# Kernel tuning notes

Measured on AMD Instinct MI355X. Metric: run time of the kernel, lower is better.

Reference implementation:

```python
import jax, jax.numpy as jnp
import numpy as np

D = 1024; H = 16; DKV = 64; DFF = 4096
NB = 32; MAXD = 128
B = 4; LD = 1024; LE = 1024
NEG = -1e9
EPS = 1e-6


def setup_inputs():
    key = jax.random.key(0)
    ks = jax.random.split(key, 13)
    s = 0.02
    def W(k, shape):
        return jax.random.normal(k, shape, jnp.float32) * s
    return {
        "encoder_hidden_states": jax.random.normal(ks[0], (B, LE, D), jnp.float32),
        "hidden_states": jax.random.normal(ks[1], (B, LD, D), jnp.float32),
        "ln1_w": jnp.ones((D,), jnp.float32),
        "sa_q": W(ks[2], (D, H * DKV)),
        "sa_k": W(ks[3], (D, H * DKV)),
        "sa_v": W(ks[4], (D, H * DKV)),
        "sa_o": W(ks[5], (H * DKV, D)),
        "rel_bias": W(ks[6], (NB, H)),
        "ln2_w": jnp.ones((D,), jnp.float32),
        "ca_q": W(ks[7], (D, H * DKV)),
        "ca_k": W(ks[8], (D, H * DKV)),
        "ca_v": W(ks[9], (D, H * DKV)),
        "ca_o": W(ks[10], (H * DKV, D)),
        "ln3_w": jnp.ones((D,), jnp.float32),
        "wi": W(ks[11], (D, DFF)),
        "wo": W(ks[12], (DFF, D)),
        "final_ln_w": jnp.ones((D,), jnp.float32),
        "encoder_attention_mask": jnp.ones((B, LE), jnp.int32),
        "attention_mask": jnp.ones((B, LD), jnp.int32),
    }


def _rms(x, w):
    # T5 LayerNorm: RMS norm, no mean subtraction, no bias
    var = jnp.mean(x * x, axis=-1, keepdims=True)
    return x * jax.lax.rsqrt(var + EPS) * w


def _rel_bucket(rp):
    # T5 relative position bucketing, non-bidirectional (decoder causal)
    n = -jnp.minimum(rp, 0)
    max_exact = NB // 2
    is_small = n < max_exact
    nf = jnp.maximum(n, 1).astype(jnp.float32)
    val_large = max_exact + (
        jnp.log(nf / max_exact) / np.log(MAXD / max_exact) * (NB - max_exact)
    ).astype(jnp.int32)
    val_large = jnp.minimum(val_large, NB - 1)
    return jnp.where(is_small, n, val_large)


def _attn(xq, xkv, Wq, Wk, Wv, Wo, bias):
    b, lq, _ = xq.shape
    lk = xkv.shape[1]
    q = (xq @ Wq).reshape(b, lq, H, DKV)
    k = (xkv @ Wk).reshape(b, lk, H, DKV)
    v = (xkv @ Wv).reshape(b, lk, H, DKV)
    # T5: no 1/sqrt(d) scaling; additive position bias + mask before softmax
    scores = jnp.einsum('bqhd,bkhd->bhqk', q, k) + bias
    p = jax.nn.softmax(scores, axis=-1)
    o = jnp.einsum('bhqk,bkhd->bqhd', p, v).reshape(b, lq, H * DKV)
    return o @ Wo


def reference(encoder_hidden_states, hidden_states, ln1_w, sa_q, sa_k, sa_v, sa_o,
              rel_bias, ln2_w, ca_q, ca_k, ca_v, ca_o, ln3_w, wi, wo, final_ln_w,
              encoder_attention_mask, attention_mask):
    b, ld, _ = hidden_states.shape
    q_pos = jnp.arange(ld)[:, None]
    k_pos = jnp.arange(ld)[None, :]
    pos_bias = rel_bias[_rel_bucket(k_pos - q_pos)].transpose(2, 0, 1)[None]  # [1,H,LD,LD]
    # decoder extended mask: causal AND padding
    self_ok = (k_pos <= q_pos)[None, None] & (attention_mask[:, None, None, :] > 0)
    self_bias = pos_bias + jnp.where(self_ok, 0.0, NEG)
    # cross-attention: encoder padding mask; enc-dec position bias is zeros
    cross_bias = jnp.where(encoder_attention_mask[:, None, None, :] > 0, 0.0, NEG)

    h = hidden_states
    x = _rms(h, ln1_w)
    h = h + _attn(x, x, sa_q, sa_k, sa_v, sa_o, self_bias)
    x = _rms(h, ln2_w)
    h = h + _attn(x, encoder_hidden_states, ca_q, ca_k, ca_v, ca_o, cross_bias)
    x = _rms(h, ln3_w)
    h = h + jax.nn.relu(x @ wi) @ wo
    return _rms(h, final_ln_w)
```

## Files before the change

kernel.cpp:

```cpp
#include <hip/hip_runtime.h>


#define BB   4
#define LDEC 1024
#define LENC 1024
#define DIM  1024
#define NH   16
#define DK   64
#define DFFN 4096
#define NEGF (-1e9f)

typedef unsigned short u16;
typedef __attribute__((ext_vector_type(8))) unsigned short u16x8;
typedef __attribute__((ext_vector_type(8))) short s16x8;
typedef __attribute__((ext_vector_type(4))) float f32x4;

__device__ __forceinline__ float bf2f(u16 u) {
    union { unsigned int i; float f; } c; c.i = ((unsigned int)u) << 16; return c.f;
}
__device__ __forceinline__ u16 f2bf(float f) {
    union { float f; unsigned int i; } c; c.f = f;
    unsigned int x = c.i;
    return (u16)((x + 0x7fffu + ((x >> 16) & 1u)) >> 16);
}
__device__ __forceinline__ bool probe_f32(const void* probe) {
    return ((const u16*)probe)[0] != 0x3F80;
}
__device__ __forceinline__ float ldx(const void* p, long i, bool f32) {
    return f32 ? ((const float*)p)[i] : bf2f(((const u16*)p)[i]);
}
__device__ __forceinline__ float4 ldx4(const void* p, long i, bool f32) {
    if (f32) return ((const float4*)p)[i >> 2];
    ushort4 u = ((const ushort4*)p)[i >> 2];
    return make_float4(bf2f(u.x), bf2f(u.y), bf2f(u.z), bf2f(u.w));
}
__device__ __forceinline__ void stx(void* p, long i, float v, bool f32) {
    if (f32) ((float*)p)[i] = v;
    else     ((u16*)p)[i] = f2bf(v);
}

__device__ __forceinline__ void gload16(const void* g, void* l) {
    __builtin_amdgcn_global_load_lds(
        (const __attribute__((address_space(1))) void*)g,
        (__attribute__((address_space(3))) void*)l, 16, 0, 0);
}

__global__ __launch_bounds__(256) void copy_k(const void* __restrict__ src,
                                              void* __restrict__ dst,
                                              const void* __restrict__ probe, int n) {
    bool pf = probe_f32(probe);
    long bytes = (long)n * (pf ? 4 : 2);
    long off = ((long)blockIdx.x * 256 + threadIdx.x) * 16;
    if (off < bytes)
        *(int4*)((char*)dst + off) = *(const int4*)((const char*)src + off);
}

__global__ __launch_bounds__(256) void cvt_k(const void* __restrict__ src,
                                             u16* __restrict__ dst,
                                             const void* __restrict__ probe, int n4) {
    bool pf = probe_f32(probe);
    int i = blockIdx.x * 256 + threadIdx.x;
    if (i >= n4) return;
    if (pf) {
        float4 f = ((const float4*)src)[i];
        ushort4 o;
        o.x = f2bf(f.x); o.y = f2bf(f.y); o.z = f2bf(f.z); o.w = f2bf(f.w);
        ((ushort4*)dst)[i] = o;
    } else {
        ((ushort4*)dst)[i] = ((const ushort4*)src)[i];
    }
}

struct TPack {
    const void* s[10]; void* d[10];
    int K[10], N[10], t0[11];
};
__global__ __launch_bounds__(256) void transp_k(TPack p, const void* __restrict__ probe) {
    bool pf = probe_f32(probe);
    __shared__ u16 tl[32][33];
    int bid = blockIdx.x;
    int w = 0;
    while (bid >= p.t0[w + 1]) ++w;
    int lt = bid - p.t0[w];
    const int K = p.K[w], N = p.N[w];
    const int ntx = N >> 5;
    const int bn = (lt % ntx) * 32, bk = (lt / ntx) * 32;
    const int c = threadIdx.x & 31, rr = threadIdx.x >> 5;
    const void* s = p.s[w];
    u16* d = (u16*)p.d[w];
#pragma unroll
    for (int i = 0; i < 4; ++i) {
        int r = rr + i * 8;
        long gi = (long)(bk + r) * N + bn + c;
        tl[c][r] = pf ? f2bf(((const float*)s)[gi]) : ((const u16*)s)[gi];
    }
    __syncthreads();
#pragma unroll
    for (int i = 0; i < 4; ++i) {
        int r = rr + i * 8;
        d[(long)(bn + r) * K + bk + c] = tl[r][c];
    }
}

template <int XM, int YM, int CP, int AD>
__global__ __launch_bounds__(256) void rms_k(const void* __restrict__ X,
                                             const void* __restrict__ w,
                                             void* __restrict__ Y,
                                             void* __restrict__ R,
                                             const u16* __restrict__ G,
                                             const u16* __restrict__ G2,
                                             const void* __restrict__ probe,
                                             long xoff, long yoff) {
    bool pf = probe_f32(probe);
    bool xf = XM && pf, yf = YM && pf;
    const int row = blockIdx.x, t = threadIdx.x;
    const long idx = (long)row * DIM + t * 4;
    float4 xv = ldx4(X, xoff + idx, xf);
    if (AD >= 1) {
        float4 gv = ldx4(G, idx, false);
        xv.x += gv.x; xv.y += gv.y; xv.z += gv.z; xv.w += gv.w;
    }
    if (AD >= 2) {
        float4 gv = ldx4(G2, idx, false);
        xv.x += gv.x; xv.y += gv.y; xv.z += gv.z; xv.w += gv.w;
    }
    float ss = xv.x * xv.x;
    ss = fmaf(xv.y, xv.y, ss);
    ss = fmaf(xv.z, xv.z, ss);
    ss = fmaf(xv.w, xv.w, ss);
#pragma unroll
    for (int off = 32; off; off >>= 1) ss += __shfl_xor(ss, off, 64);
    __shared__ float part[4];
    if ((t & 63) == 0) part[t >> 6] = ss;
    __syncthreads();
    float tot = part[0] + part[1] + part[2] + part[3];
    float scale = rsqrtf(tot * (1.f / (float)DIM) + 1e-6f);
    float4 wv = ldx4(w, t * 4, pf);
    if (CP) {
        stx(R, idx + 0, xv.x, pf);
        stx(R, idx + 1, xv.y, pf);
        stx(R, idx + 2, xv.z, pf);
        stx(R, idx + 3, xv.w, pf);
    }
    stx(Y, yoff + idx + 0, xv.x * scale * wv.x, yf);
    stx(Y, yoff + idx + 1, xv.y * scale * wv.y, yf);
    stx(Y, yoff + idx + 2, xv.z * scale * wv.z, yf);
    stx(Y, yoff + idx + 3, xv.w * scale * wv.w, yf);
}

struct Gemm2Arg {
    const u16* A; const u16* BT; void* C;
    long aoff; long boff; long coff; int ldb; int klen;
};

template <int EPI, int BM>
__global__ __launch_bounds__(512) void mgemm2_k(Gemm2Arg g0, Gemm2Arg g1, Gemm2Arg g2,
                                                const void* __restrict__ probe,
                                                int M, int N, int K) {
    const bool pf = probe_f32(probe);
    Gemm2Arg ga = (blockIdx.z == 0) ? g0 : (blockIdx.z == 1 ? g1 : g2);
    constexpr int AG = BM / 64;
    constexpr int AFR = BM / 32;

    __shared__ u16 Asm[2][BM * 64];
    __shared__ u16 Bsm[2][128 * 64];

    const int tid = threadIdx.x;
    const int nx = gridDim.x;
    const int nwg = nx * gridDim.y;
    const int L = blockIdx.x + nx * blockIdx.y;
    const int tile = (L & 7) * (nwg >> 3) + (L >> 3);
    const int m_base = (tile / nx) * BM, n_base = (tile % nx) * 128;

    const int w = tid >> 6, lane = tid & 63;
    const int wm = w >> 2, wn = w & 3;
    const int l15 = lane & 15, quad = lane >> 4;
    const int arow8 = lane >> 3;
    const int acg = (lane & 7) ^ arow8;

    const int iters = ga.klen >> 6;
    const u16* Ab = ga.A + ga.aoff;
    const u16* Bb = ga.BT + ga.boff;

#pragma unroll
    for (int g = 0; g < AG; ++g)
        gload16(Ab + (long)(m_base + w * (BM / 8) + g * 8 + arow8) * K + acg * 8,
                &Asm[0][(w * (BM / 8) + g * 8) * 64]);
#pragma unroll
    for (int g = 0; g < 2; ++g)
        gload16(Bb + (long)(n_base + w * 16 + g * 8 + arow8) * ga.ldb + acg * 8,
                &Bsm[0][(w * 16 + g * 8) * 64]);

    f32x4 acc[AFR][2] = {};
    int cur = 0;
    for (int it = 0; it < iters; ++it) {
        __syncthreads();
        if (it + 1 < iters) {
            const int k0 = (it + 1) << 6;
#pragma unroll
            for (int g = 0; g < AG; ++g)
                gload16(Ab + (long)(m_base + w * (BM / 8) + g * 8 + arow8) * K + k0 + acg * 8,
                        &Asm[cur ^ 1][(w * (BM / 8) + g * 8) * 64]);
#pragma unroll
            for (int g = 0; g < 2; ++g)
                gload16(Bb + (long)(n_base + w * 16 + g * 8 + arow8) * ga.ldb + k0 + acg * 8,
                        &Bsm[cur ^ 1][(w * 16 + g * 8) * 64]);
        }
#pragma unroll
        for (int s = 0; s < 2; ++s) {
            s16x8 afr[AFR], bfr[2];
#pragma unroll
            for (int i = 0; i < AFR; ++i) {
                int row = wm * (BM / 2) + i * 16 + l15;
                int chunk = ((s << 2) | quad) ^ (row & 7);
                afr[i] = *(const s16x8*)&Asm[cur][row * 64 + chunk * 8];
            }
#pragma unroll
            for (int j = 0; j < 2; ++j) {
                int nr = wn * 32 + j * 16 + l15;
                int chunk = ((s << 2) | quad) ^ (nr & 7);
                bfr[j] = *(const s16x8*)&Bsm[cur][nr * 64 + chunk * 8];
            }
#pragma unroll
            for (int i = 0; i < AFR; ++i)
#pragma unroll
                for (int j = 0; j < 2; ++j)
                    acc[i][j] = __builtin_amdgcn_mfma_f32_16x16x32_bf16(
                        afr[i], bfr[j], acc[i][j], 0, 0, 0);
        }
        cur ^= 1;
    }

#pragma unroll
    for (int i = 0; i < AFR; ++i) {
#pragma unroll
        for (int j = 0; j < 2; ++j) {
            int n = n_base + wn * 32 + j * 16 + l15;
#pragma unroll
            for (int r4 = 0; r4 < 4; ++r4) {
                int m = m_base + wm * (BM / 2) + i * 16 + quad * 4 + r4;
                float v = acc[i][j][r4];
                if (EPI == 1) v = fmaxf(v, 0.f);
                long cidx = ga.coff + (long)m * N + n;
                if (EPI == 2) {
                    v += ldx(ga.C, cidx, pf);
                    stx(ga.C, cidx, v, pf);
                } else {
                    ((u16*)ga.C)[cidx] = f2bf(v);
                }
            }
        }
    }
}

struct GemmArg {
    const void* A; const void* B; void* C;
    long aoff; long boff; long coff; int asrc; int bsrc; int ldb;
};

__device__ __forceinline__ void load_breg(const GemmArg& ga, bool bf, int k0,
                                          int bk2, int bnb, int n_base, u16* breg) {
    long base0 = (long)(k0 + bk2) * ga.ldb + ga.boff + n_base + bnb;
    long base1 = base0 + ga.ldb;
    if (bf) {
        const float4* Bf = (const float4*)ga.B;
#pragma unroll
        for (int r = 0; r < 2; ++r) {
            long b = (r ? base1 : base0) >> 2;
#pragma unroll
            for (int c = 0; c < 2; ++c) {
                float4 f = Bf[b + c];
                breg[r * 8 + c * 4 + 0] = f2bf(f.x);
                breg[r * 8 + c * 4 + 1] = f2bf(f.y);
                breg[r * 8 + c * 4 + 2] = f2bf(f.z);
                breg[r * 8 + c * 4 + 3] = f2bf(f.w);
            }
        }
    } else {
        u16x8 v0 = *(const u16x8*)((const u16*)ga.B + base0);
        u16x8 v1 = *(const u16x8*)((const u16*)ga.B + base1);
#pragma unroll
        for (int i = 0; i < 8; ++i) { breg[i] = v0[i]; breg[8 + i] = v1[i]; }
    }
}

template <int EPI>
__global__ __launch_bounds__(512) void mgemm_k(GemmArg g0, GemmArg g1, GemmArg g2,
                                               const void* __restrict__ probe,
                                               int M, int N, int K) {
    const bool pf = probe_f32(probe);
    GemmArg ga = (blockIdx.z == 0) ? g0 : (blockIdx.z == 1 ? g1 : g2);
    const bool af = (ga.asrc >= 1) && pf;
    const bool bf = (ga.bsrc >= 1) && pf;

    __shared__ u16 Asm[2][128 * 64];
    __shared__ u16 Bsm[128 * 64];

    const int tid = threadIdx.x;
    const int nx = gridDim.x;
    const int nwg = nx * gridDim.y;
    const int L = blockIdx.x + nx * blockIdx.y;
    const int tile = (L & 7) * (nwg >> 3) + (L >> 3);
    const int m_base = (tile / nx) * 128, n_base = (tile % nx) * 128;

    const int w = tid >> 6, lane = tid & 63;
    const int wm = w >> 2, wn = w & 3;
    const int l15 = lane & 15, quad = lane >> 4;

    const int bk2 = (tid & 31) * 2;
    const int bnb = (tid >> 5) * 8;
    const int arow8 = lane >> 3;
    const int acg = (lane & 7) ^ arow8;

    const int iters = K >> 6;
    u16 breg[16];
    load_breg(ga, bf, 0, bk2, bnb, n_base, breg);
    if (!af) {
#pragma unroll
        for (int g = 0; g < 2; ++g) {
            const u16* Ag = (const u16*)ga.A + ga.aoff +
                            (long)(m_base + w * 16 + g * 8 + arow8) * K + acg * 8;
            gload16(Ag, &Asm[0][(w * 16 + g * 8) * 64]);
        }
    }

    f32x4 acc[4][2] = {};

    for (int it = 0; it < iters; ++it) {
        const int cur = it & 1;
        __syncthreads();
        if (af) {
            const int row = tid >> 2;
            const float4* Af = (const float4*)ga.A;
            long gb = ga.aoff + (long)(m_base + row) * K + (it << 6);
#pragma unroll
            for (int c = 0; c < 2; ++c) {
                int cg = (tid & 3) * 2 + c;
                float4 fa = Af[(gb + cg * 8) >> 2];
                float4 fb = Af[((gb + cg * 8) >> 2) + 1];
                u16x8 o;
                o[0] = f2bf(fa.x); o[1] = f2bf(fa.y); o[2] = f2bf(fa.z); o[3] = f2bf(fa.w);
                o[4] = f2bf(fb.x); o[5] = f2bf(fb.y); o[6] = f2bf(fb.z); o[7] = f2bf(fb.w);
                *(u16x8*)&Asm[cur][row * 64 + ((cg ^ (row & 7)) << 3)] = o;
            }
        }
#pragma unroll
        for (int i = 0; i < 8; ++i) {
            int n = bnb + i;
            unsigned int pr = (unsigned int)breg[i] | ((unsigned int)breg[8 + i] << 16);
            *(unsigned int*)&Bsm[n * 64 + (((bk2 >> 3) ^ (n & 7)) << 3) + (bk2 & 7)] = pr;
        }
        __syncthreads();
        if (it + 1 < iters) {
            load_breg(ga, bf, (it + 1) << 6, bk2, bnb, n_base, breg);
            if (!af) {
#pragma unroll
                for (int g = 0; g < 2; ++g) {
                    const u16* Ag = (const u16*)ga.A + ga.aoff +
                                    (long)(m_base + w * 16 + g * 8 + arow8) * K +
                                    ((it + 1) << 6) + acg * 8;
                    gload16(Ag, &Asm[cur ^ 1][(w * 16 + g * 8) * 64]);
                }
            }
        }
#pragma unroll
        for (int s = 0; s < 2; ++s) {
            s16x8 afr[4], bfr[2];
#pragma unroll
            for (int i = 0; i < 4; ++i) {
                int row = wm * 64 + i * 16 + l15;
                int chunk = ((s << 2) | quad) ^ (row & 7);
                afr[i] = *(const s16x8*)&Asm[cur][row * 64 + chunk * 8];
            }
#pragma unroll
            for (int j = 0; j < 2; ++j) {
                int nr = wn * 32 + j * 16 + l15;
                int chunk = ((s << 2) | quad) ^ (nr & 7);
                bfr[j] = *(const s16x8*)&Bsm[nr * 64 + chunk * 8];
            }
#pragma unroll
            for (int i = 0; i < 4; ++i)
#pragma unroll
                for (int j = 0; j < 2; ++j)
                    acc[i][j] = __builtin_amdgcn_mfma_f32_16x16x32_bf16(
                        afr[i], bfr[j], acc[i][j], 0, 0, 0);
        }
    }

#pragma unroll
    for (int i = 0; i < 4; ++i) {
#pragma unroll
        for (int j = 0; j < 2; ++j) {
            int n = n_base + wn * 32 + j * 16 + l15;
#pragma unroll
            for (int r4 = 0; r4 < 4; ++r4) {
                int m = m_base + wm * 64 + i * 16 + quad * 4 + r4;
                float v = acc[i][j][r4];
                if (EPI == 1) v = fmaxf(v, 0.f);
                long cidx = ga.coff + (long)m * N + n;
                if (EPI == 2) {
                    v += ldx(ga.C, cidx, pf);
                    stx(ga.C, cidx, v, pf);
                } else {
                    ((u16*)ga.C)[cidx] = f2bf(v);
                }
            }
        }
    }
}

template <int SELF>
__global__ __launch_bounds__(256) void fattn_k(const u16* __restrict__ Q,
                                               const u16* __restrict__ K,
                                               const u16* __restrict__ V,
                                               const void* __restrict__ relb,
                                               const int* __restrict__ mask,
                                               u16* __restrict__ O,
                                               const void* __restrict__ probe,
                                               int LK, int b0, int bufrows) {
    const bool pf = probe_f32(probe);
    __shared__ u16 Ks[64][72];
    __shared__ u16 Vt[64][72];
    __shared__ u16 Ps[64][72];
    __shared__ float bias_lut[SELF ? 1024 : 1];

    const int t = threadIdx.x;
    const int lane = t & 63, w = t >> 6;
    const int l15 = lane & 15, quad = lane >> 4;

    int x, h, z;
    if (gridDim.z == 4) {
        int lid = blockIdx.x + (int)gridDim.x * (blockIdx.y + (int)gridDim.y * blockIdx.z);
        int q = lid >> 8, r = lid & 255, a = r & 3;
        x = (q == 0) ? a : (q == 1) ? 15 - a : (q == 2) ? 4 + a : 11 - a;
        h = (r >> 2) & 15;
        z = r >> 6;
    } else {
        x = blockIdx.x; h = blockIdx.y; z = blockIdx.z;
    }
    const int q0 = x * 64;
    const int batch = b0 + z;
    const long bv = (long)z * bufrows * DIM;
    const int* mrow = mask + batch * LK;

    if (SELF) {
        for (int i = t; i < 1024; i += 256) {
            int bucket;
            if (i < 16) bucket = i;
            else {
                int vv = 16 + (int)(logf((float)i * 0.0625f) * 7.69436394f);
                bucket = vv < 31 ? vv : 31;
            }
            bias_lut[i] = ldx(relb, bucket * NH + h, pf);
        }
    }

    s16x8 qf[2];
    {
        const u16* qp = Q + bv + (long)(q0 + w * 16 + l15) * DIM + h * DK + quad * 8;
        qf[0] = *(const s16x8*)qp;
        qf[1] = *(const s16x8*)(qp + 32);
    }

    float l_reg[4] = {0.f, 0.f, 0.f, 0.f};
    f32x4 Oa[4] = {};

    const int ntiles = SELF ? (q0 >> 6) + 1 : (LK >> 6);
    const int kr = t >> 2, kseg = t & 3;
    const int kr2 = (t & 31) * 2, dnb = (t >> 5) * 8;

    u16x8 kp0, kp1, vp0, vp1;
    {
        long gb = bv + (long)kr * DIM + h * DK + kseg * 16;
        kp0 = *(const u16x8*)(K + gb);
        kp1 = *(const u16x8*)(K + gb + 8);
        long gv = bv + (long)kr2 * DIM + h * DK + dnb;
        vp0 = *(const u16x8*)(V + gv);
        vp1 = *(const u16x8*)(V + gv + DIM);
    }

    for (int kt = 0; kt < ntiles; ++kt) {
        __syncthreads();
        *(u16x8*)&Ks[kr][kseg * 16] = kp0;
        *(u16x8*)&Ks[kr][kseg * 16 + 8] = kp1;
#pragma unroll
        for (int i = 0; i < 8; ++i) {
            unsigned int pr = (unsigned int)vp0[i] | ((unsigned int)vp1[i] << 16);
            *(unsigned int*)&Vt[dnb + i][kr2] = pr;
        }
        __syncthreads();
        if (kt + 1 < ntiles) {
            long gb = bv + (long)((kt + 1) * 64 + kr) * DIM + h * DK + kseg * 16;
            kp0 = *(const u16x8*)(K + gb);
            kp1 = *(const u16x8*)(K + gb + 8);
            long gv = bv + (long)((kt + 1) * 64 + kr2) * DIM + h * DK + dnb;
            vp0 = *(const u16x8*)(V + gv);
            vp1 = *(const u16x8*)(V + gv + DIM);
        }

        f32x4 sc[4] = {};
        __builtin_amdgcn_s_setprio(1);
#pragma unroll
        for (int j = 0; j < 4; ++j)
#pragma unroll
            for (int s = 0; s < 2; ++s) {
                s16x8 bf = *(const s16x8*)&Ks[j * 16 + l15][s * 32 + quad * 8];
                sc[j] = __builtin_amdgcn_mfma_f32_16x16x32_bf16(qf[s], bf, sc[j], 0, 0, 0);
            }
        __builtin_amdgcn_s_setprio(0);

#pragma unroll
        for (int j = 0; j < 4; ++j) {
            int key = kt * 64 + j * 16 + l15;
            float ma = (mrow[key] > 0) ? 0.f : NEGF;
#pragma unroll
            for (int r = 0; r < 4; ++r) {
                float sv = sc[j][r];
                if (SELF) {
                    int q = q0 + w * 16 + quad * 4 + r;
                    int d = q - key;
                    sv += bias_lut[d < 0 ? 0 : d] + ((key <= q) ? ma : NEGF);
                } else {
                    sv += ma;
                }
                float p = __expf(sv);
                Ps[w * 16 + quad * 4 + r][j * 16 + l15] = f2bf(p);
                l_reg[r] += p;
            }
        }
        asm volatile("" ::: "memory");

        __builtin_amdgcn_s_setprio(1);
#pragma unroll
        for (int s = 0; s < 2; ++s) {
            s16x8 pa = *(const s16x8*)&Ps[w * 16 + l15][s * 32 + quad * 8];
#pragma unroll
            for (int j = 0; j < 4; ++j) {
                s16x8 vb = *(const s16x8*)&Vt[j * 16 + l15][s * 32 + quad * 8];
                Oa[j] = __builtin_amdgcn_mfma_f32_16x16x32_bf16(pa, vb, Oa[j], 0, 0, 0);
            }
        }
        __builtin_amdgcn_s_setprio(0);
    }

#pragma unroll
    for (int r = 0; r < 4; ++r) {
        float v = l_reg[r];
        v += __shfl_xor(v, 1, 64);
        v += __shfl_xor(v, 2, 64);
        v += __shfl_xor(v, 4, 64);
        v += __shfl_xor(v, 8, 64);
        l_reg[r] = 1.f / v;
    }
#pragma unroll
    for (int j = 0; j < 4; ++j)
#pragma unroll
        for (int r = 0; r < 4; ++r) {
            int row = w * 16 + quad * 4 + r;
            O[bv + (long)(q0 + row) * DIM + h * DK + j * 16 + l15] =
                f2bf(Oa[j][r] * l_reg[r]);
        }
}

extern "C" void kernel_launch(void* const* d_in, const int* in_sizes, int n_in,
                              void* d_out, int out_size, void* d_ws, size_t ws_size,
                              hipStream_t stream) {
    const void* enc  = d_in[0];
    const void* hs   = d_in[1];
    const void* ln1  = d_in[2];
    const void* sa_q = d_in[3];
    const void* sa_k = d_in[4];
    const void* sa_v = d_in[5];
    const void* sa_o = d_in[6];
    const void* relb = d_in[7];
    const void* ln2  = d_in[8];
    const void* ca_q = d_in[9];
    const void* ca_k = d_in[10];
    const void* ca_v = d_in[11];
    const void* ca_o = d_in[12];
    const void* ln3  = d_in[13];
    const void* wi   = d_in[14];
    const void* wo   = d_in[15];
    const void* fln  = d_in[16];
    const int* enc_mask = (const int*)d_in[17];
    const int* dec_mask = (const int*)d_in[18];
    void* out = d_out;
    const void* probe = ln1;

    char* ws = (char*)d_ws;
    const int M = BB * LDEC;
    dim3 blk(256), blkG(512);
    GemmArg dz = {nullptr, nullptr, nullptr, 0, 0, 0, 0, 0, 0};
    Gemm2Arg dz2 = {nullptr, nullptr, nullptr, 0, 0, 0, 0, 0};

    if (ws_size >= (72ull << 20)) {
        u16* X0 = (u16*)(ws);
        u16* X1 = (u16*)(ws + (8u  << 20));
        u16* X2 = (u16*)(ws + (16u << 20));
        u16* X3 = (u16*)(ws + (24u << 20));
        u16* FF = X1;
        u16* encB = (u16*)(ws + (32u << 20));
        u16* G3b = (u16*)(ws + (40u << 20));
        u16* wT[10];
        wT[0] = (u16*)(ws + (40u << 20));
        wT[1] = (u16*)(ws + (42u << 20));
        wT[2] = (u16*)(ws + (44u << 20));
        wT[3] = (u16*)(ws + (46u << 20));
        wT[4] = (u16*)(ws + (48u << 20));
        wT[5] = (u16*)(ws + (50u << 20));
        wT[6] = (u16*)(ws + (52u << 20));
        wT[7] = (u16*)(ws + (54u << 20));
        wT[8] = (u16*)(ws + (56u << 20));
        wT[9] = (u16*)(ws + (64u << 20));

        cvt_k<<<4096, blk, 0, stream>>>(enc, encB, probe, 1048576);
        {
            TPack p;
            const void* s[10] = {sa_q, sa_k, sa_v, sa_o, ca_q, ca_k, ca_v, ca_o, wi, wo};
            const int kk[10] = {DIM, DIM, DIM, DIM, DIM, DIM, DIM, DIM, DIM, DFFN};
            const int nn[10] = {DIM, DIM, DIM, DIM, DIM, DIM, DIM, DIM, DFFN, DIM};
            int acc = 0;
            for (int i = 0; i < 10; ++i) {
                p.s[i] = s[i]; p.d[i] = wT[i]; p.K[i] = kk[i]; p.N[i] = nn[i];
                p.t0[i] = acc; acc += (kk[i] >> 5) * (nn[i] >> 5);
            }
            p.t0[10] = acc;
            transp_k<<<acc, blk, 0, stream>>>(p, probe);
        }

        dim3 gQKV(8, 64, 3);
        dim3 gOP2(8, 64, 2);
        dim3 gWI(16, 64, 2);
        dim3 gAttn(LDEC / 64, NH, BB);

        rms_k<1, 0, 1, 0><<<M, blk, 0, stream>>>(hs, ln1, X0, out, nullptr, nullptr,
                                                 probe, 0, 0);
        {
            Gemm2Arg zq = {X0, wT[0], X1, 0, 0, 0, DIM, DIM};
            Gemm2Arg zk = {X0, wT[1], X2, 0, 0, 0, DIM, DIM};
            Gemm2Arg zv = {X0, wT[2], X3, 0, 0, 0, DIM, DIM};
            mgemm2_k<0, 64><<<gQKV, blkG, 0, stream>>>(zq, zk, zv, probe, M, DIM, DIM);
        }
        fattn_k<1><<<gAttn, blk, 0, stream>>>(X1, X2, X3, relb, dec_mask, X0,
                                              probe, LDEC, 0, LDEC);
        {
            Gemm2Arg za = {X0, wT[3], X1, 0, 0, 0, DIM, 512};
            Gemm2Arg zb = {X0, wT[3], X2, 512, 512, 0, DIM, 512};
            mgemm2_k<0, 64><<<gOP2, blkG, 0, stream>>>(za, zb, dz2, probe, M, DIM, DIM);
        }

        rms_k<1, 0, 1, 2><<<M, blk, 0, stream>>>(out, ln2, X0, out, X1, X2,
                                                 probe, 0, 0);
        {
            Gemm2Arg zq = {X0, wT[4], X1, 0, 0, 0, DIM, DIM};
            Gemm2Arg zk = {encB, wT[5], X2, 0, 0, 0, DIM, DIM};
            Gemm2Arg zv = {encB, wT[6], X3, 0, 0, 0, DIM, DIM};
            mgemm2_k<0, 64><<<gQKV, blkG, 0, stream>>>(zq, zk, zv, probe, M, DIM, DIM);
        }
        fattn_k<0><<<gAttn, blk, 0, stream>>>(X1, X2, X3, relb, enc_mask, X0,
                                              probe, LENC, 0, LENC);
        {
            Gemm2Arg za = {X0, wT[7], X1, 0, 0, 0, DIM, 512};
            Gemm2Arg zb = {X0, wT[7], X2, 512, 512, 0, DIM, 512};
            mgemm2_k<0, 64><<<gOP2, blkG, 0, stream>>>(za, zb, dz2, probe, M, DIM, DIM);
        }

        rms_k<1, 0, 1, 2><<<M, blk, 0, stream>>>(out, ln3, X0, out, X1, X2,
                                                 probe, 0, 0);
        {
            Gemm2Arg z0 = {X0, wT[8], FF, 0, 0, 0, DIM, DIM};
            Gemm2Arg z1 = {X0, wT[8], FF, 0, (long)2048 * DIM, 2048, DIM, DIM};
            mgemm2_k<1, 64><<<gWI, blkG, 0, stream>>>(z0, z1, dz2, probe, M, DFFN, DIM);
        }
        {
            Gemm2Arg za = {FF, wT[9], X0, 0, 0, 0, DFFN, 2048};
            Gemm2Arg zb = {FF, wT[9], G3b, 2048, 2048, 0, DFFN, 2048};
            mgemm2_k<0, 64><<<gOP2, blkG, 0, stream>>>(za, zb, dz2, probe, M, DIM, DFFN);
        }

        rms_k<1, 1, 0, 2><<<M, blk, 0, stream>>>(out, fln, out, nullptr, X0, G3b,
                                                 probe, 0, 0);
    } else if (ws_size >= (32ull << 20)) {
        u16* X0 = (u16*)(ws);
        u16* X1 = (u16*)(ws + (8u << 20));
        u16* X2 = (u16*)(ws + (16u << 20));
        u16* X3 = (u16*)(ws + (24u << 20));
        u16* FF = X2;
        const bool have_encb = ws_size >= (40ull << 20);
        u16* encB = (u16*)(ws + (32u << 20));

        dim3 gQKV(8, 32, 3);
        dim3 gOP(8, 32, 1);
        dim3 gWI(16, 32, 1);
        dim3 gAttn(LDEC / 64, NH, BB);

        copy_k<<<(M * DIM / 4) / 256, blk, 0, stream>>>(hs, out, probe, M * DIM);
        if (have_encb)
            cvt_k<<<4096, blk, 0, stream>>>(enc, encB, probe, M * DIM / 4);

        rms_k<1, 0, 0, 0><<<M, blk, 0, stream>>>(out, ln1, X0, nullptr, nullptr, nullptr, probe, 0, 0);
        {
            GemmArg zq = {X0, sa_q, X1, 0, 0, 0, 0, 1, DIM};
            GemmArg zk = {X0, sa_k, X2, 0, 0, 0, 0, 1, DIM};
            GemmArg zv = {X0, sa_v, X3, 0, 0, 0, 0, 1, DIM};
            mgemm_k<0><<<gQKV, blkG, 0, stream>>>(zq, zk, zv, probe, M, DIM, DIM);
        }
        fattn_k<1><<<gAttn, blk, 0, stream>>>(X1, X2, X3, relb, dec_mask, X0,
                                              probe, LDEC, 0, LDEC);
        {
            GemmArg zo = {X0, sa_o, out, 0, 0, 0, 0, 1, DIM};
            mgemm_k<2><<<gOP, blkG, 0, stream>>>(zo, dz, dz, probe, M, DIM, DIM);
        }

        rms_k<1, 0, 0, 0><<<M, blk, 0, stream>>>(out, ln2, X0, nullptr, nullptr, nullptr, probe, 0, 0);
        {
            const void* encA = have_encb ? (const void*)encB : enc;
            int asrc = have_encb ? 0 : 1;
            GemmArg zq = {X0, ca_q, X1, 0, 0, 0, 0, 1, DIM};
            GemmArg zk = {encA, ca_k, X2, 0, 0, 0, asrc, 1, DIM};
            GemmArg zv = {encA, ca_v, X3, 0, 0, 0, asrc, 1, DIM};
            mgemm_k<0><<<gQKV, blkG, 0, stream>>>(zq, zk, zv, probe, M, DIM, DIM);
        }
        fattn_k<0><<<gAttn, blk, 0, stream>>>(X1, X2, X3, relb, enc_mask, X0,
                                              probe, LENC, 0, LENC);
        {
            GemmArg zo = {X0, ca_o, out, 0, 0, 0, 0, 1, DIM};
            mgemm_k<2><<<gOP, blkG, 0, stream>>>(zo, dz, dz, probe, M, DIM, DIM);
        }

        rms_k<1, 0, 0, 0><<<M, blk, 0, stream>>>(out, ln3, X0, nullptr, nullptr, nullptr, probe, 0, 0);
        for (int d = 0; d < 2; ++d) {
            GemmArg zi = {X0, wi, FF, 0, (long)d * 2048, 0, 0, 1, DFFN};
            mgemm_k<1><<<gWI, blkG, 0, stream>>>(zi, dz, dz, probe, M, 2048, DIM);
            GemmArg zo = {FF, wo, out, 0, (long)d * 2048 * DIM, 0, 0, 1, DIM};
            mgemm_k<2><<<gOP, blkG, 0, stream>>>(zo, dz, dz, probe, M, DIM, 2048);
        }
        rms_k<1, 1, 0, 0><<<M, blk, 0, stream>>>(out, fln, out, nullptr, nullptr, nullptr, probe, 0, 0);
        return;
    } else {
        u16* X0 = (u16*)(ws);
        u16* X1 = (u16*)(ws + (2u << 20));
        u16* X2 = (u16*)(ws + (4u << 20));
        u16* X3 = (u16*)(ws + (6u << 20));
        u16* XN = (u16*)(ws);
        u16* FF = (u16*)(ws + (4u << 20));
        dim3 gQKV(8, 8, 3);
        dim3 gOP(8, 8, 1);
        dim3 gFFN(8, 16, 1);
        dim3 gAttn(LDEC / 64, NH, 1);

        copy_k<<<(M * DIM / 4) / 256, blk, 0, stream>>>(hs, out, probe, M * DIM);

        for (int b = 0; b < BB; ++b) {
            const long ob = (long)b * LDEC * DIM;
            const long eb = (long)b * LENC * DIM;

            rms_k<1, 0, 0, 0><<<LDEC, blk, 0, stream>>>(out, ln1, X0, nullptr, nullptr, nullptr, probe, ob, 0);
            {
                GemmArg zq = {X0, sa_q, X1, 0, 0, 0, 0, 1, DIM};
                GemmArg zk = {X0, sa_k, X2, 0, 0, 0, 0, 1, DIM};
                GemmArg zv = {X0, sa_v, X3, 0, 0, 0, 0, 1, DIM};
                mgemm_k<0><<<gQKV, blkG, 0, stream>>>(zq, zk, zv, probe, LDEC, DIM, DIM);
            }
            fattn_k<1><<<gAttn, blk, 0, stream>>>(X1, X2, X3, relb, dec_mask, X0,
                                                  probe, LDEC, b, 0);
            {
                GemmArg zo = {X0, sa_o, out, 0, 0, ob, 0, 1, DIM};
                mgemm_k<2><<<gOP, blkG, 0, stream>>>(zo, dz, dz, probe, LDEC, DIM, DIM);
            }

            rms_k<1, 0, 0, 0><<<LDEC, blk, 0, stream>>>(out, ln2, X0, nullptr, nullptr, nullptr, probe, ob, 0);
            {
                GemmArg zq = {X0, ca_q, X1, 0, 0, 0, 0, 1, DIM};
                GemmArg zk = {enc, ca_k, X2, eb, 0, 0, 1, 1, DIM};
                GemmArg zv = {enc, ca_v, X3, eb, 0, 0, 1, 1, DIM};
                mgemm_k<0><<<gQKV, blkG, 0, stream>>>(zq, zk, zv, probe, LENC, DIM, DIM);
            }
            fattn_k<0><<<gAttn, blk, 0, stream>>>(X1, X2, X3, relb, enc_mask, X0,
                                                  probe, LENC, b, 0);
            {
                GemmArg zo = {X0, ca_o, out, 0, 0, ob, 0, 1, DIM};
                mgemm_k<2><<<gOP, blkG, 0, stream>>>(zo, dz, dz, probe, LDEC, DIM, DIM);
            }
        }

        for (int mc = 0; mc < 2; ++mc) {
            const long r0 = (long)mc * 2048;
            rms_k<1, 0, 0, 0><<<2048, blk, 0, stream>>>(out, ln3, XN, nullptr, nullptr, nullptr, probe, r0 * DIM, 0);
            for (int d = 0; d < 4; ++d) {
                GemmArg zi = {XN, wi, FF, 0, (long)d * 1024, 0, 0, 1, DFFN};
                mgemm_k<1><<<gFFN, blkG, 0, stream>>>(zi, dz, dz, probe, 2048, 1024, DIM);
                GemmArg zo = {FF, wo, out, 0, (long)d * 1024 * DIM, r0 * DIM, 0, 1, DIM};
                mgemm_k<2><<<gFFN, blkG, 0, stream>>>(zo, dz, dz, probe, 2048, DIM, 1024);
            }
        }
        rms_k<1, 1, 0, 0><<<M, blk, 0, stream>>>(out, fln, out, nullptr, nullptr, nullptr, probe, 0, 0);
        return;
    }
}
```

Measured before the change: 500.8 us.

## Vectorize weight transpose and drop split-K for FFN output GEMM

```diff
diff --git a/kernel.cpp b/kernel.cpp
--- a/kernel.cpp
+++ b/kernel.cpp
@@ -77,7 +77,7 @@
 };
 __global__ __launch_bounds__(256) void transp_k(TPack p, const void* __restrict__ probe) {
     bool pf = probe_f32(probe);
-    __shared__ u16 tl[32][33];
+    __shared__ u16 tl[32][36];
     int bid = blockIdx.x;
     int w = 0;
     while (bid >= p.t0[w + 1]) ++w;
@@ -85,21 +85,29 @@
     const int K = p.K[w], N = p.N[w];
     const int ntx = N >> 5;
     const int bn = (lt % ntx) * 32, bk = (lt / ntx) * 32;
-    const int c = threadIdx.x & 31, rr = threadIdx.x >> 5;
+    const int r0 = threadIdx.x >> 3;
+    const int cg = threadIdx.x & 7;
     const void* s = p.s[w];
     u16* d = (u16*)p.d[w];
-#pragma unroll
-    for (int i = 0; i < 4; ++i) {
-        int r = rr + i * 8;
-        long gi = (long)(bk + r) * N + bn + c;
-        tl[c][r] = pf ? f2bf(((const float*)s)[gi]) : ((const u16*)s)[gi];
+    {
+        long gi = (long)(bk + r0) * N + bn + cg * 4;
+        if (pf) {
+            float4 f = ((const float4*)s)[gi >> 2];
+            tl[cg * 4 + 0][r0] = f2bf(f.x);
+            tl[cg * 4 + 1][r0] = f2bf(f.y);
+            tl[cg * 4 + 2][r0] = f2bf(f.z);
+            tl[cg * 4 + 3][r0] = f2bf(f.w);
+        } else {
+            ushort4 u = ((const ushort4*)s)[gi >> 2];
+            tl[cg * 4 + 0][r0] = u.x;
+            tl[cg * 4 + 1][r0] = u.y;
+            tl[cg * 4 + 2][r0] = u.z;
+            tl[cg * 4 + 3][r0] = u.w;
+        }
     }
     __syncthreads();
-#pragma unroll
-    for (int i = 0; i < 4; ++i) {
-        int r = rr + i * 8;
-        d[(long)(bn + r) * K + bk + c] = tl[r][c];
-    }
+    ushort4 o = *(const ushort4*)&tl[r0][cg * 4];
+    *(ushort4*)&d[(long)(bn + r0) * K + bk + cg * 4] = o;
 }
 
 template <int XM, int YM, int CP, int AD>
@@ -600,7 +608,6 @@
         u16* X3 = (u16*)(ws + (24u << 20));
         u16* FF = X1;
         u16* encB = (u16*)(ws + (32u << 20));
-        u16* G3b = (u16*)(ws + (40u << 20));
         u16* wT[10];
         wT[0] = (u16*)(ws + (40u << 20));
         wT[1] = (u16*)(ws + (42u << 20));
@@ -629,6 +636,7 @@
         }
 
         dim3 gQKV(8, 64, 3);
+        dim3 gOP(8, 64, 1);
         dim3 gOP2(8, 64, 2);
         dim3 gWI(16, 64, 2);
         dim3 gAttn(LDEC / 64, NH, BB);
@@ -673,12 +681,11 @@
             mgemm2_k<1, 64><<<gWI, blkG, 0, stream>>>(z0, z1, dz2, probe, M, DFFN, DIM);
         }
         {
-            Gemm2Arg za = {FF, wT[9], X0, 0, 0, 0, DFFN, 2048};
-            Gemm2Arg zb = {FF, wT[9], G3b, 2048, 2048, 0, DFFN, 2048};
-            mgemm2_k<0, 64><<<gOP2, blkG, 0, stream>>>(za, zb, dz2, probe, M, DIM, DFFN);
-        }
-
-        rms_k<1, 1, 0, 2><<<M, blk, 0, stream>>>(out, fln, out, nullptr, X0, G3b,
+            Gemm2Arg zo = {FF, wT[9], X0, 0, 0, 0, DFFN, DFFN};
+            mgemm2_k<0, 64><<<gOP, blkG, 0, stream>>>(zo, dz2, dz2, probe, M, DIM, DFFN);
+        }
+
+        rms_k<1, 1, 0, 1><<<M, blk, 0, stream>>>(out, fln, out, nullptr, X0, nullptr,
                                                  probe, 0, 0);
     } else if (ws_size >= (32ull << 20)) {
         u16* X0 = (u16*)(ws);
```

New measurement: 490.7 us. 2.0% less time.
